# Kernel optimization log

Measured on AMD Instinct MI355X. Metric: run time of the kernel, lower is better.

Reference implementation:

```python
import jax, jax.numpy as jnp
import numpy as np
from jax.scipy.linalg import solve_triangular

B, L, D, H = 1, 2048, 1024, 4
DK = DV = D // H  # 256
CONV = 4
FIR_S, FIR_M, FIR_L = 3, 15, 63
CHUNK = 32


def _l2norm(x):
    return x * jax.lax.rsqrt(jnp.sum(x * x, -1, keepdims=True) + 1e-6)


def _short_conv(x, w):
    # depthwise causal conv1d (fla ShortConvolution) + silu; x:(B,L,C), w:(C,K)
    K = w.shape[-1]
    l = x.shape[1]
    xp = jnp.pad(x, ((0, 0), (K - 1, 0), (0, 0)))
    y = sum(xp[:, j:j + l, :] * w[:, j] for j in range(K))
    return jax.nn.silu(y)


def _fir(x, filt):
    # DepthwiseFIRConv1d: x:(B,L,H,Dv), filt:(H,Dv,K), causal depthwise conv
    b, l, h, d = x.shape
    K = filt.shape[-1]
    xf = jnp.transpose(x.reshape(b, l, h * d), (0, 2, 1))  # (B, C, L)
    y = jax.lax.conv_general_dilated(xf, filt.reshape(h * d, 1, K), (1,), [(K - 1, 0)],
                                     feature_group_count=h * d)
    return jnp.transpose(y, (0, 2, 1)).reshape(b, l, h, d)


def _delta_rule_chunkwise(q, k, v, beta):
    # q,k:(B,H,L,dk)  v:(B,H,L,dv)  beta:(B,H,L); L divisible by CHUNK
    b, h, Lq, dk = q.shape
    c = CHUNK
    n = Lq // c
    q = _l2norm(q)
    k = _l2norm(k)
    v = v * beta[..., None]
    kb = k * beta[..., None]
    rs = lambda t: t.reshape(b, h, n, c, t.shape[-1])
    qc, kc, vc, kbc = rs(q), rs(k), rs(v), rs(kb)
    # per-chunk UT transform: attn_inv = (I - strictly_lower(-(kb k^T)))^{-1}
    tri_strict = jnp.tril(jnp.ones((c, c), bool), -1)
    A = jnp.where(tri_strict, -(kbc @ jnp.swapaxes(kc, -1, -2)), 0.0)  # (B,H,n,c,c)
    eye = jnp.eye(c, dtype=q.dtype)
    M = eye - A  # unit lower triangular
    T = solve_triangular(M, jnp.broadcast_to(eye, M.shape), lower=True)
    u = T @ vc   # (B,H,n,c,dv)
    w = T @ kbc  # (B,H,n,c,dk)
    causal = jnp.tril(jnp.ones((c, c), bool))  # include diagonal

    def step(S, inp):
        q_i, k_i, u_i, w_i = inp
        attn = jnp.where(causal, q_i @ jnp.swapaxes(k_i, -1, -2), 0.0)
        u_adj = u_i - w_i @ S
        o_i = q_i @ S + attn @ u_adj
        return S + jnp.swapaxes(k_i, -1, -2) @ u_adj, o_i

    S0 = jnp.zeros((b, h, dk, v.shape[-1]), q.dtype)
    mv = lambda t: jnp.moveaxis(t, 2, 0)  # chunk axis to scan axis
    _, o = jax.lax.scan(step, S0, (mv(qc), mv(kc), mv(u), mv(w)))
    return jnp.moveaxis(o, 0, 2).reshape(b, h, Lq, -1)


def _rmsnorm(x, w, eps=1e-5):
    return x * jax.lax.rsqrt(jnp.mean(x * x, -1, keepdims=True) + eps) * w


def setup_inputs() -> dict:
    key = jax.random.key(0)
    ks = jax.random.split(key, 16)
    wn = lambda k, shape, s: jax.random.normal(k, shape, jnp.float32) * s

    def fir_init(k, K):
        f = jnp.zeros((H, DV, K), jnp.float32).at[..., -1].set(1.0)  # delta kernel
        return f + wn(k, (H, DV, K), 0.01)

    return {
        "hidden_states": jax.random.normal(ks[0], (B, L, D), jnp.float32),
        "Wq": wn(ks[1], (D, D), 0.02),
        "Wk": wn(ks[2], (D, D), 0.02),
        "Wv": wn(ks[3], (D, D), 0.02),
        "Wb": wn(ks[4], (H, D), 0.02),
        "conv_q": wn(ks[5], (D, CONV), 0.1),
        "conv_k": wn(ks[6], (D, CONV), 0.1),
        "conv_v": wn(ks[7], (D, CONV), 0.1),
        "fir_s": fir_init(ks[8], FIR_S),
        "fir_m": fir_init(ks[9], FIR_M),
        "fir_l": fir_init(ks[10], FIR_L),
        "gate_w": wn(ks[11], (H, 5, D), 1.0 / np.sqrt(D)),
        "gate_b": jnp.zeros((H, 5), jnp.float32),
        "log_temp": jnp.zeros((H, 1), jnp.float32),
        "eps_param": jnp.full((H, 1), 0.02, jnp.float32),
        "norm_w": jnp.ones((DV,), jnp.float32),
        "Wo": wn(ks[12], (D, D), 0.02),
    }


def reference(hidden_states, Wq, Wk, Wv, Wb, conv_q, conv_k, conv_v,
              fir_s, fir_m, fir_l, gate_w, gate_b, log_temp, eps_param,
              norm_w, Wo):
    b, l, d = hidden_states.shape
    # projections + short conv (silu activation, qk_activation='silu')
    q = _short_conv(hidden_states @ Wq.T, conv_q).reshape(b, l, H, DK)
    k = _short_conv(hidden_states @ Wk.T, conv_k).reshape(b, l, H, DK)
    v_direct = _short_conv(hidden_states @ Wv.T, conv_v).reshape(b, l, H, DV)
    beta = jax.nn.sigmoid(hidden_states @ Wb.T)  # (B,L,H)
    tp = lambda t: jnp.transpose(t, (0, 2, 1, 3))
    delta_out = tp(_delta_rule_chunkwise(tp(q), tp(k), tp(v_direct),
                                         jnp.transpose(beta, (0, 2, 1))))
    local_s = _fir(v_direct, fir_s)
    local_m = _fir(v_direct, fir_m)
    local_l = _fir(v_direct, fir_l)
    # per-head 5-way gate with temperature + eps floor
    logits = jnp.einsum('bld,hpd->blhp', hidden_states, gate_w) + gate_b
    temp = jnp.exp(log_temp).reshape(1, 1, H, 1)
    probs = jax.nn.softmax(logits / temp, -1)
    eps = jnp.clip(eps_param, 0.0, 0.2).reshape(1, 1, H, 1)
    probs = probs * (1.0 - 5.0 * eps) + eps
    o = (probs[..., 0:1] * local_s + probs[..., 1:2] * local_m +
         probs[..., 2:3] * local_l + probs[..., 3:4] * delta_out +
         probs[..., 4:5] * v_direct)
    o = _rmsnorm(o, norm_w)  # per-head RMSNorm (use_gate=False)
    return o.reshape(b, l, H * DV) @ Wo.T
```

## Files before the change

### kernel.cpp

```cpp
#include <hip/hip_runtime.h>

#define LSEQ 2048
#define DMOD 1024
#define NH   4
#define DH   256
#define NCH  64
#define CPAD 260

typedef unsigned short u16;
typedef short bf16x8 __attribute__((ext_vector_type(8)));
typedef float f32x4  __attribute__((ext_vector_type(4)));

#define MFMA16(a,b,c) __builtin_amdgcn_mfma_f32_16x16x32_bf16((a),(b),(c),0,0,0)

__device__ __forceinline__ float sigf(float x){ return 1.0f/(1.0f + expf(-x)); }

__device__ __forceinline__ u16 f2bf(float f){
  unsigned u = __float_as_uint(f);
  return (u16)((u + 0x7FFFu + ((u>>16)&1u)) >> 16);
}
__device__ __forceinline__ unsigned pk2(float a, float b){
  return (unsigned)f2bf(a) | ((unsigned)f2bf(b) << 16);
}
__device__ __forceinline__ float bf2f(u16 x){ return __uint_as_float(((unsigned)x)<<16); }

__device__ __forceinline__ void stage16(const void* g, void* l){
  __builtin_amdgcn_global_load_lds((const __attribute__((address_space(1))) unsigned*)g,
                                   (__attribute__((address_space(3))) unsigned*)l, 16, 0, 0);
}

__global__ __launch_bounds__(256) void cvt_all(
    const float* __restrict__ hidden, const float* __restrict__ Wq,
    const float* __restrict__ Wk, const float* __restrict__ Wv,
    const float* __restrict__ Wo, u16* __restrict__ hidb,
    u16* __restrict__ wqkvb, u16* __restrict__ wob)
{
  const int i4 = blockIdx.x*256 + threadIdx.x;
  const int e = i4*4;
  const float* src; u16* dst; int off;
  if (e < 2*1048576)      { src = hidden; dst = hidb;  off = e; }
  else if (e < 3*1048576) { src = Wq; dst = wqkvb; off = e - 2*1048576; }
  else if (e < 4*1048576) { src = Wk; dst = wqkvb + 1048576; off = e - 3*1048576; }
  else if (e < 5*1048576) { src = Wv; dst = wqkvb + 2*1048576; off = e - 4*1048576; }
  else                    { src = Wo; dst = wob; off = e - 5*1048576; }
  float4 v = *(const float4*)(src + off);
  *(uint2*)(dst + off) = make_uint2(pk2(v.x,v.y), pk2(v.z,v.w));
}

__global__ __launch_bounds__(256) void gemm_qkv(
    const u16* __restrict__ A, const u16* __restrict__ B,
    float* __restrict__ Cq, float* __restrict__ Ck, float* __restrict__ Cv)
{
  __shared__ __align__(16) u16 Asl[2][128][32];
  __shared__ __align__(16) u16 Bsl[2][128][32];
  const int i0 = blockIdx.x*128, j0 = blockIdx.y*128;
  const int t = threadIdx.x, lane = t & 63, wv = t >> 6;
  const int wm = wv >> 1, wn = wv & 1;
  const int li = lane & 15, g = lane >> 4;
  const int lr = lane >> 2, lc = lane & 3;
  f32x4 acc[4][4] = {};

  auto stageAB = [&](int buf, int kt){
    const int k0 = kt*32;
    #pragma unroll
    for (int c2=0;c2<2;c2++){
      const int row = wv*32 + c2*16 + lr;
      stage16(A + (size_t)(i0+row)*1024 + k0 + lc*8, &Asl[buf][wv*32 + c2*16][0]);
      stage16(B + (size_t)(j0+row)*1024 + k0 + lc*8, &Bsl[buf][wv*32 + c2*16][0]);
    }
  };

  int buf = 0;
  stageAB(0, 0);
  for (int kt=0; kt<32; kt++){
    __syncthreads();
    if (kt+1 < 32) stageAB(buf^1, kt+1);
    bf16x8 af[4], bf[4];
    #pragma unroll
    for (int mt=0;mt<4;mt++) af[mt] = *(const bf16x8*)&Asl[buf][wm*64+mt*16+li][g*8];
    #pragma unroll
    for (int nt=0;nt<4;nt++) bf[nt] = *(const bf16x8*)&Bsl[buf][wn*64+nt*16+li][g*8];
    #pragma unroll
    for (int mt=0;mt<4;mt++)
      #pragma unroll
      for (int nt=0;nt<4;nt++)
        acc[mt][nt] = MFMA16(af[mt], bf[nt], acc[mt][nt]);
    buf ^= 1;
  }
  float* C = (blockIdx.y < 8) ? Cq : (blockIdx.y < 16) ? Ck : Cv;
  const int jl = j0 & 1023;
  #pragma unroll
  for (int mt=0;mt<4;mt++){
    #pragma unroll
    for (int nt=0;nt<4;nt++){
      #pragma unroll
      for (int r=0;r<4;r++){
        const int row = i0 + wm*64 + mt*16 + g*4 + r;
        const int col = jl + wn*64 + nt*16 + li;
        C[(size_t)row*1024 + col] = acc[mt][nt][r];
      }
    }
  }
}

__global__ __launch_bounds__(256) void gemm_bf16(
    const u16* __restrict__ A, const u16* __restrict__ B,
    float* __restrict__ C, int M, int N, int K)
{
  __shared__ __align__(16) u16 Asl[2][128][32];
  __shared__ __align__(16) u16 Bsl[2][128][32];
  const int i0 = blockIdx.x*128, j0 = blockIdx.y*128;
  const int t = threadIdx.x, lane = t & 63, wv = t >> 6;
  const int wm = wv >> 1, wn = wv & 1;
  const int li = lane & 15, g = lane >> 4;
  const int lr = lane >> 2, lc = lane & 3;
  f32x4 acc[4][4] = {};

  auto stageAB = [&](int buf, int kt){
    const int k0 = kt*32;
    #pragma unroll
    for (int c2=0;c2<2;c2++){
      const int row = wv*32 + c2*16 + lr;
      stage16(A + (size_t)(i0+row)*K + k0 + lc*8, &Asl[buf][wv*32 + c2*16][0]);
      stage16(B + (size_t)(j0+row)*K + k0 + lc*8, &Bsl[buf][wv*32 + c2*16][0]);
    }
  };

  int buf = 0;
  const int nk = K/32;
  stageAB(0, 0);
  for (int kt=0; kt<nk; kt++){
    __syncthreads();
    if (kt+1 < nk) stageAB(buf^1, kt+1);
    bf16x8 af[4], bf[4];
    #pragma unroll
    for (int mt=0;mt<4;mt++) af[mt] = *(const bf16x8*)&Asl[buf][wm*64+mt*16+li][g*8];
    #pragma unroll
    for (int nt=0;nt<4;nt++) bf[nt] = *(const bf16x8*)&Bsl[buf][wn*64+nt*16+li][g*8];
    #pragma unroll
    for (int mt=0;mt<4;mt++)
      #pragma unroll
      for (int nt=0;nt<4;nt++)
        acc[mt][nt] = MFMA16(af[mt], bf[nt], acc[mt][nt]);
    buf ^= 1;
  }
  #pragma unroll
  for (int mt=0;mt<4;mt++){
    #pragma unroll
    for (int nt=0;nt<4;nt++){
      #pragma unroll
      for (int r=0;r<4;r++){
        const int row = i0 + wm*64 + mt*16 + g*4 + r;
        const int col = j0 + wn*64 + nt*16 + li;
        C[(size_t)row*N + col] = acc[mt][nt][r];
      }
    }
  }
}

__global__ __launch_bounds__(256) void conv_silu3(
    const float* __restrict__ tq, const float* __restrict__ tk, const float* __restrict__ tv,
    const float* __restrict__ wq, const float* __restrict__ wk, const float* __restrict__ wv2,
    u16* __restrict__ oq, u16* __restrict__ ok, u16* __restrict__ ov)
{
  const int idx = blockIdx.x*256 + threadIdx.x;
  const int which = idx >> 21;
  const int lidx = idx & ((1<<21)-1);
  const float* x = (which==0) ? tq : (which==1) ? tk : tv;
  const float* w = (which==0) ? wq : (which==1) ? wk : wv2;
  u16* y = (which==0) ? oq : (which==1) ? ok : ov;
  const int c = lidx & (DMOD-1);
  const int i = lidx >> 10;
  float4 wc = *(const float4*)(w + (size_t)c*4);
  float acc = wc.w * x[lidx];
  if (i >= 1) acc += wc.z * x[lidx -   DMOD];
  if (i >= 2) acc += wc.y * x[lidx - 2*DMOD];
  if (i >= 3) acc += wc.x * x[lidx - 3*DMOD];
  y[lidx] = f2bf(acc * sigf(acc));
}

__global__ __launch_bounds__(256) void beta_gate(
    const float* __restrict__ hidden, const float* __restrict__ Wb,
    const float* __restrict__ gw, const float* __restrict__ gb,
    const float* __restrict__ logtemp, const float* __restrict__ epsp,
    float* __restrict__ betab, float* __restrict__ probs)
{
  const int i = blockIdx.x, t = threadIdx.x;
  float4 h4 = *(const float4*)(hidden + (size_t)i*DMOD + t*4);
  float part[24];
  #pragma unroll
  for (int o=0;o<24;o++){
    const float* wr = (o<4) ? (Wb + (size_t)o*DMOD) : (gw + (size_t)(o-4)*DMOD);
    float4 w4 = *(const float4*)(wr + t*4);
    part[o] = h4.x*w4.x + h4.y*w4.y + h4.z*w4.z + h4.w*w4.w;
  }
  __shared__ float red[24][4];
  __shared__ float fin[24];
  const int lane = t & 63, wv = t >> 6;
  #pragma unroll
  for (int o=0;o<24;o++){
    float vv = part[o];
    #pragma unroll
    for (int m=1;m<64;m<<=1) vv += __shfl_xor(vv, m, 64);
    if (lane == 0) red[o][wv] = vv;
  }
  __syncthreads();
  if (t < 24) fin[t] = red[t][0]+red[t][1]+red[t][2]+red[t][3];
  __syncthreads();
  if (t < NH){
    const int hh = t;
    betab[(size_t)i*NH + hh] = sigf(fin[hh]);
    float temp = expf(logtemp[hh]);
    float lg[5], mx = -1e30f;
    #pragma unroll
    for (int p=0;p<5;p++){ lg[p] = (fin[4+hh*5+p] + gb[hh*5+p]) / temp; mx = fmaxf(mx, lg[p]); }
    float ex[5], s = 0.f;
    #pragma unroll
    for (int p=0;p<5;p++){ ex[p] = expf(lg[p]-mx); s += ex[p]; }
    float eps = fminf(fmaxf(epsp[hh], 0.f), 0.2f);
    #pragma unroll
    for (int p=0;p<5;p++) probs[((size_t)i*NH+hh)*5 + p] = (ex[p]/s)*(1.f-5.f*eps) + eps;
  }
}

__global__ __launch_bounds__(256) void delta_pre(
    const u16* __restrict__ q, const u16* __restrict__ k, const u16* __restrict__ v,
    const float* __restrict__ beta,
    u16* __restrict__ qbg, u16* __restrict__ wng, u16* __restrict__ kTg,
    u16* __restrict__ atg, float* __restrict__ ubuf)
{
  const int n = blockIdx.x, h = blockIdx.y;
  const int t = threadIdx.x;
  __shared__ float q_s[32][CPAD], k_s[32][CPAD], v_s[32][CPAD];
  __shared__ float T_s[32][32], Tb_s[32][32], M_s[32][32];
  __shared__ float rr[2][32][8];
  __shared__ float scl[2][32];
  __shared__ float bet_s[32];

  const int row = t >> 3, cq = t & 7;
  const size_t gb = (size_t)(n*32+row)*DMOD + h*DH + cq*32;
  const size_t cb = (size_t)(h*NCH+n)*32*256;
  const int sw = (row & 7) << 3;
  float psq = 0.f, psk = 0.f;
  #pragma unroll
  for (int x=0;x<4;x++){
    uint4 qa = *(const uint4*)(q + gb + x*8);
    uint4 ka = *(const uint4*)(k + gb + x*8);
    uint4 va = *(const uint4*)(v + gb + x*8);
    const unsigned qw[4] = {qa.x,qa.y,qa.z,qa.w};
    const unsigned kw[4] = {ka.x,ka.y,ka.z,ka.w};
    const unsigned vw[4] = {va.x,va.y,va.z,va.w};
    #pragma unroll
    for (int e=0;e<4;e++){
      float q0 = bf2f((u16)(qw[e]&0xffff)), q1 = bf2f((u16)(qw[e]>>16));
      float k0 = bf2f((u16)(kw[e]&0xffff)), k1 = bf2f((u16)(kw[e]>>16));
      float v0 = bf2f((u16)(vw[e]&0xffff)), v1 = bf2f((u16)(vw[e]>>16));
      q_s[row][cq*32+x*8+e*2]   = q0; q_s[row][cq*32+x*8+e*2+1] = q1;
      k_s[row][cq*32+x*8+e*2]   = k0; k_s[row][cq*32+x*8+e*2+1] = k1;
      v_s[row][cq*32+x*8+e*2]   = v0; v_s[row][cq*32+x*8+e*2+1] = v1;
      psq += q0*q0 + q1*q1;
      psk += k0*k0 + k1*k1;
    }
  }
  rr[0][row][cq] = psq; rr[1][row][cq] = psk;
  if (t < 32) bet_s[t] = beta[(size_t)(n*32+t)*NH + h];
  __syncthreads();
  if (t < 64){
    const int wh = t >> 5, r = t & 31;
    float s = 1e-6f;
    #pragma unroll
    for (int x=0;x<8;x++) s += rr[wh][r][x];
    scl[wh][r] = rsqrtf(s);
  }
  __syncthreads();
  {
    const float sq = scl[0][row], sk2 = scl[1][row];
    #pragma unroll
    for (int x=0;x<8;x++){
      float4 qa = *(float4*)&q_s[row][cq*32+x*4];
      qa.x*=sq; qa.y*=sq; qa.z*=sq; qa.w*=sq;
      *(float4*)&q_s[row][cq*32+x*4] = qa;
      *(uint2*)&qbg[cb + (size_t)row*256 + ((cq*32 + x*4) ^ sw)] =
          make_uint2(pk2(qa.x,qa.y), pk2(qa.z,qa.w));
      float4 ka = *(float4*)&k_s[row][cq*32+x*4];
      ka.x*=sk2; ka.y*=sk2; ka.z*=sk2; ka.w*=sk2;
      *(float4*)&k_s[row][cq*32+x*4] = ka;
    }
  }
  __syncthreads();
  {
    unsigned* kp = (unsigned*)(kTg + ((size_t)(h*NCH+n)*256 + t)*32);
    #pragma unroll
    for (int c2=0;c2<16;c2++)
      kp[c2 ^ ((t&3)<<2)] = pk2(k_s[2*c2][t], k_s[2*c2+1][t]);
  }
  {
    const int c = t >> 3, m0 = (t & 7)*4;
    float d0=0.f,d1=0.f,d2=0.f,d3=0.f;
    for (int kk=0;kk<DH;kk+=4){
      float4 a  = *(const float4*)&k_s[c][kk];
      float4 b0 = *(const float4*)&k_s[m0+0][kk];
      float4 b1 = *(const float4*)&k_s[m0+1][kk];
      float4 b2 = *(const float4*)&k_s[m0+2][kk];
      float4 b3 = *(const float4*)&k_s[m0+3][kk];
      d0 += a.x*b0.x + a.y*b0.y + a.z*b0.z + a.w*b0.w;
      d1 += a.x*b1.x + a.y*b1.y + a.z*b1.z + a.w*b1.w;
      d2 += a.x*b2.x + a.y*b2.y + a.z*b2.z + a.w*b2.w;
      d3 += a.x*b3.x + a.y*b3.y + a.z*b3.z + a.w*b3.w;
    }
    const float bc = bet_s[c];
    M_s[c][m0+0] = (m0+0 < c) ? bc*d0 : ((m0+0==c)?1.f:0.f);
    M_s[c][m0+1] = (m0+1 < c) ? bc*d1 : ((m0+1==c)?1.f:0.f);
    M_s[c][m0+2] = (m0+2 < c) ? bc*d2 : ((m0+2==c)?1.f:0.f);
    M_s[c][m0+3] = (m0+3 < c) ? bc*d3 : ((m0+3==c)?1.f:0.f);
  }
  __syncthreads();
  if (t < 32){
    const int j = t;
    for (int c=0;c<32;c++){
      float s = (c==j) ? 1.f : 0.f;
      for (int m=0;m<c;m++) s -= M_s[c][m]*T_s[m][j];
      T_s[c][j] = s;
    }
  }
  __syncthreads();
  {
    const int c = t >> 3, m0 = (t & 7)*4;
    #pragma unroll
    for (int x=0;x<4;x++) Tb_s[c][m0+x] = T_s[c][m0+x]*bet_s[m0+x];
  }
  __syncthreads();
  {
    const int colb = (t & 7)*4;
    float4 aw[8] = {};
    float4 au[8] = {};
    for (int m=0;m<32;m++){
      const float tb = Tb_s[row][m];
      #pragma unroll
      for (int y=0;y<8;y++){
        float4 kv = *(const float4*)&k_s[m][colb + y*32];
        float4 vv = *(const float4*)&v_s[m][colb + y*32];
        aw[y].x += tb*kv.x; aw[y].y += tb*kv.y; aw[y].z += tb*kv.z; aw[y].w += tb*kv.w;
        au[y].x += tb*vv.x; au[y].y += tb*vv.y; au[y].z += tb*vv.z; au[y].w += tb*vv.w;
      }
    }
    const size_t ob = (size_t)(n*32+row)*DMOD + h*DH + colb;
    #pragma unroll
    for (int y=0;y<8;y++){
      *(uint2*)&wng[cb + (size_t)row*256 + ((colb + y*32) ^ sw)] =
          make_uint2(pk2(-aw[y].x,-aw[y].y), pk2(-aw[y].z,-aw[y].w));
      *(float4*)(ubuf + ob + y*32) = au[y];
    }
  }
  {
    const int c = t >> 3, m0 = (t & 7)*4;
    float d0=0.f,d1=0.f,d2=0.f,d3=0.f;
    for (int kk=0;kk<DH;kk+=4){
      float4 a  = *(const float4*)&q_s[c][kk];
      float4 b0 = *(const float4*)&k_s[m0+0][kk];
      float4 b1 = *(const float4*)&k_s[m0+1][kk];
      float4 b2 = *(const float4*)&k_s[m0+2][kk];
      float4 b3 = *(const float4*)&k_s[m0+3][kk];
      d0 += a.x*b0.x + a.y*b0.y + a.z*b0.z + a.w*b0.w;
      d1 += a.x*b1.x + a.y*b1.y + a.z*b1.z + a.w*b1.w;
      d2 += a.x*b2.x + a.y*b2.y + a.z*b2.z + a.w*b2.w;
      d3 += a.x*b3.x + a.y*b3.y + a.z*b3.z + a.w*b3.w;
    }
    d0 = (m0+0 <= c) ? d0 : 0.f;
    d1 = (m0+1 <= c) ? d1 : 0.f;
    d2 = (m0+2 <= c) ? d2 : 0.f;
    d3 = (m0+3 <= c) ? d3 : 0.f;
    *(uint2*)&atg[((size_t)(h*NCH+n)*32 + c)*32 + (m0 ^ ((c&3)<<3))] =
        make_uint2(pk2(d0,d1), pk2(d2,d3));
  }
}

__global__ __launch_bounds__(256) void delta_scan_fused(
    const u16* __restrict__ qbg, const u16* __restrict__ wng,
    const u16* __restrict__ kTg, const u16* __restrict__ atg,
    const float* __restrict__ ubuf, float* __restrict__ dob)
{
  const int qd = blockIdx.x, h = blockIdx.y;
  const int t = threadIdx.x, lane = t & 63, wv = t >> 6;
  const int cs = wv & 1, j = wv >> 1;
  const int g = lane >> 4, li = lane & 15;
  const int swz = (li & 7) << 3;
  const int kswz = (li & 3) << 3;

  __shared__ __align__(16) unsigned char stg[2][53248];
  __shared__ __align__(16) u16 ST[16][264];
  __shared__ __align__(16) u16 uaT[16][40];
  __shared__ __align__(16) float pfo[2][2][64][4];

  f32x4 S[4];
  #pragma unroll
  for (int i=0;i<4;i++) S[i] = (f32x4){0.f,0.f,0.f,0.f};
  for (int i=t; i<16*264; i+=256) (&ST[0][0])[i] = 0;

  auto issue_stage = [&](int nn, int b){
    char* L = (char*)&stg[b][0];
    const size_t cbB = (size_t)(h*NCH+nn)*16384;
    #pragma unroll
    for (int jj=0;jj<13;jj++){
      const int s = wv*13 + jj;
      if (s < 48){
        const char* gsc = (s<16) ? (const char*)wng + cbB + (size_t)s*1024
                       : (s<32) ? (const char*)qbg + cbB + (size_t)(s-16)*1024
                                : (const char*)kTg + cbB + (size_t)(s-32)*1024;
        stage16(gsc + (size_t)lane*16, L + s*1024);
      } else if (s < 50){
        stage16((const char*)atg + (size_t)(h*NCH+nn)*2048 + (size_t)(s-48)*1024 + (size_t)lane*16,
                L + 49152 + (s-48)*1024);
      } else {
        const int i2 = s - 50;
        stage16(ubuf + (size_t)(nn*32 + i2*16 + (lane>>2))*DMOD + h*DH + qd*16 + (lane&3)*4,
                L + 51200 + i2*1024);
      }
    }
  };

  issue_stage(0, 0);

  for (int n=0;n<NCH;n++){
    const int b = n & 1;
    if (n == 0) asm volatile("s_waitcnt vmcnt(0)" ::: "memory");
    else        asm volatile("s_waitcnt vmcnt(2)" ::: "memory");
    asm volatile("s_waitcnt lgkmcnt(0)" ::: "memory");
    __builtin_amdgcn_s_barrier();
    __builtin_amdgcn_sched_barrier(0);
    issue_stage((n+1 < NCH) ? n+1 : NCH-1, b^1);

    const char* L = (const char*)&stg[b][0];
    const u16*  wl = (const u16*)(L);
    const u16*  ql = (const u16*)(L + 16384);
    const u16*  kl = (const u16*)(L + 32768);
    const u16*  al = (const u16*)(L + 49152);
    const float* ul = (const float*)(L + 51200);

    bf16x8 Bs[8];
    #pragma unroll
    for (int kb=0;kb<8;kb++)
      Bs[kb] = *(const bf16x8*)&ST[li][kb*32 + g*8];

    f32x4 ua;
    #pragma unroll
    for (int r=0;r<4;r++)
      ua[r] = ul[(cs*16 + g*4 + r)*16 + li];
    f32x4 x2 = (f32x4){0.f,0.f,0.f,0.f};
    #pragma unroll
    for (int kb=0;kb<4;kb++){
      const int idx = (kb*32 + g*8) ^ swz;
      bf16x8 aw = *(const bf16x8*)&wl[(size_t)(cs*16+li)*256 + idx];
      ua = MFMA16(aw, Bs[kb], ua);
    }
    #pragma unroll
    for (int kb=4;kb<8;kb++){
      const int idx = (kb*32 + g*8) ^ swz;
      bf16x8 aw = *(const bf16x8*)&wl[(size_t)(cs*16+li)*256 + idx];
      x2 = MFMA16(aw, Bs[kb], x2);
    }
    #pragma unroll
    for (int r=0;r<4;r++) ua[r] += x2[r];

    f32x4 op = (f32x4){0.f,0.f,0.f,0.f};
    if (j == 0){
      #pragma unroll
      for (int kb=0;kb<4;kb++){
        const int idx = (kb*32 + g*8) ^ swz;
        bf16x8 aq = *(const bf16x8*)&ql[(size_t)(cs*16+li)*256 + idx];
        op = MFMA16(aq, Bs[kb], op);
      }
    } else {
      #pragma unroll
      for (int kb2=0;kb2<4;kb2++){
        const int idx = ((4+kb2)*32 + g*8) ^ swz;
        bf16x8 aq = *(const bf16x8*)&ql[(size_t)(cs*16+li)*256 + idx];
        op = MFMA16(aq, Bs[4+kb2], op);
      }
    }
    *(f32x4*)&pfo[j][cs][lane][0] = op;

    if (j == 0) *(unsigned*)&uaT[li][cs*16 + g*4]     = pk2(ua[0], ua[1]);
    else        *(unsigned*)&uaT[li][cs*16 + g*4 + 2] = pk2(ua[2], ua[3]);
    asm volatile("s_waitcnt lgkmcnt(0)" ::: "memory");
    __builtin_amdgcn_s_barrier();
    __builtin_amdgcn_sched_barrier(0);

    bf16x8 bu = *(const bf16x8*)&uaT[li][g*8];

    #pragma unroll
    for (int mtl=0;mtl<4;mtl++){
      const int rowk = (wv*4+mtl)*16 + li;
      bf16x8 a = *(const bf16x8*)&kl[(size_t)rowk*32 + ((g*8) ^ kswz)];
      S[mtl] = MFMA16(a, bu, S[mtl]);
    }
    #pragma unroll
    for (int mtl=0;mtl<4;mtl++)
      *(uint2*)&ST[li][(wv*4+mtl)*16 + g*4] =
          make_uint2(pk2(S[mtl][0],S[mtl][1]), pk2(S[mtl][2],S[mtl][3]));

    f32x4 atp = (f32x4){0.f,0.f,0.f,0.f};
    {
      bf16x8 a = *(const bf16x8*)&al[(size_t)(cs*16+li)*32 + ((g*8) ^ kswz)];
      atp = MFMA16(a, bu, atp);
    }

    {
      f32x4 oq = *(const f32x4*)&pfo[j^1][cs][lane][0];
      const size_t ob = (size_t)(n*32 + cs*16)*DMOD + h*DH + qd*16 + li;
      if (j == 0){
        dob[ob + (size_t)(g*4+0)*DMOD] = op[0] + oq[0] + atp[0];
        dob[ob + (size_t)(g*4+1)*DMOD] = op[1] + oq[1] + atp[1];
      } else {
        dob[ob + (size_t)(g*4+2)*DMOD] = op[2] + oq[2] + atp[2];
        dob[ob + (size_t)(g*4+3)*DMOD] = op[3] + oq[3] + atp[3];
      }
    }
  }
}

__global__ void prep_fir(const float* __restrict__ fs, const float* __restrict__ fm,
                         const float* __restrict__ fl, float* __restrict__ fts,
                         float* __restrict__ ftm, float* __restrict__ ftl)
{
  const int idx = blockIdx.x*256 + threadIdx.x;
  if (idx < 63*1024){
    const int j = idx >> 10, c = idx & 1023;
    ftl[idx] = fl[(size_t)c*63 + j];
  } else if (idx < 78*1024){
    const int r = idx - 63*1024;
    const int j = r >> 10, c = r & 1023;
    ftm[r] = fm[(size_t)c*15 + j];
  } else {
    const int r = idx - 78*1024;
    const int j = r >> 10, c = r & 1023;
    fts[r] = fs[(size_t)c*3 + j];
  }
}

__global__ __launch_bounds__(256) void fir_mix(
    const u16* __restrict__ vb, const float* __restrict__ dout,
    const float* __restrict__ probs, const float* __restrict__ ftl,
    const float* __restrict__ ftm, const float* __restrict__ fts,
    const float* __restrict__ normw, u16* __restrict__ omixb)
{
  const int i0 = blockIdx.x*16, h = blockIdx.y;
  const int t = threadIdx.x;
  const int c = h*DH + t;
  __shared__ float vwin[78][256];
  __shared__ float red[16][4];

  for (int ll=0; ll<78; ll++){
    const int row = i0 - 62 + ll;
    vwin[ll][t] = (row >= 0) ? bf2f(vb[(size_t)row*DMOD + c]) : 0.f;
  }
  __syncthreads();

  float mixv[16];
  #pragma unroll
  for (int cch=0; cch<4; cch++){
    float as[4] = {0,0,0,0}, am[4] = {0,0,0,0}, alg[4] = {0,0,0,0};
    for (int jt=0; jt<63; jt++){
      const float f = ftl[(size_t)jt*DMOD + c];
      #pragma unroll
      for (int q2=0;q2<4;q2++) alg[q2] += f * vwin[cch*4+q2 + jt][t];
    }
    #pragma unroll
    for (int jt=0; jt<15; jt++){
      const float f = ftm[(size_t)jt*DMOD + c];
      #pragma unroll
      for (int q2=0;q2<4;q2++) am[q2] += f * vwin[cch*4+q2 + 48 + jt][t];
    }
    #pragma unroll
    for (int jt=0; jt<3; jt++){
      const float f = fts[(size_t)jt*DMOD + c];
      #pragma unroll
      for (int q2=0;q2<4;q2++) as[q2] += f * vwin[cch*4+q2 + 60 + jt][t];
    }
    #pragma unroll
    for (int q2=0;q2<4;q2++){
      const int ii = cch*4+q2;
      const int i = i0+ii;
      const float* pr = probs + ((size_t)i*NH + h)*5;
      const float dvv = dout[(size_t)i*DMOD + c];
      const float vv  = vwin[62+ii][t];
      mixv[ii] = pr[0]*as[q2] + pr[1]*am[q2] + pr[2]*alg[q2] + pr[3]*dvv + pr[4]*vv;
    }
  }
  const int lane = t & 63, wvw = t >> 6;
  #pragma unroll
  for (int ii=0;ii<16;ii++){
    float ss = mixv[ii]*mixv[ii];
    #pragma unroll
    for (int m=1;m<64;m<<=1) ss += __shfl_xor(ss, m, 64);
    if (lane == 0) red[ii][wvw] = ss;
  }
  __syncthreads();
  #pragma unroll
  for (int ii=0;ii<16;ii++){
    const float tot = red[ii][0]+red[ii][1]+red[ii][2]+red[ii][3];
    const float o = mixv[ii] * rsqrtf(tot*(1.f/256.f) + 1e-5f) * normw[t];
    omixb[(size_t)(i0+ii)*DMOD + c] = f2bf(o);
  }
}

extern "C" void kernel_launch(void* const* d_in, const int* in_sizes, int n_in,
                              void* d_out, int out_size, void* d_ws, size_t ws_size,
                              hipStream_t stream)
{
  const float* hidden = (const float*)d_in[0];
  const float* Wq     = (const float*)d_in[1];
  const float* Wk     = (const float*)d_in[2];
  const float* Wv     = (const float*)d_in[3];
  const float* Wb     = (const float*)d_in[4];
  const float* convq  = (const float*)d_in[5];
  const float* convk  = (const float*)d_in[6];
  const float* convv  = (const float*)d_in[7];
  const float* firs   = (const float*)d_in[8];
  const float* firm   = (const float*)d_in[9];
  const float* firl   = (const float*)d_in[10];
  const float* gatew  = (const float*)d_in[11];
  const float* gateb  = (const float*)d_in[12];
  const float* logtemp= (const float*)d_in[13];
  const float* epsp   = (const float*)d_in[14];
  const float* normw  = (const float*)d_in[15];
  const float* Wo     = (const float*)d_in[16];
  float* out = (float*)d_out;

  char* W = (char*)d_ws;
  const size_t MB = (size_t)1 << 20;
  float* tmpq  = (float*)(W + 0*MB);
  float* dob   = (float*)(W + 0*MB);
  float* tmpk  = (float*)(W + 8*MB);
  float* ubuf  = (float*)(W + 8*MB);
  float* tmpv  = (float*)(W + 16*MB);
  u16*   omixb = (u16*)  (W + 16*MB);
  u16*   qb    = (u16*)  (W + 24*MB);
  u16*   kb    = (u16*)  (W + 28*MB);
  u16*   vb    = (u16*)  (W + 32*MB);
  u16*   hidb  = (u16*)  (W + 36*MB);
  u16*   wqkvb = (u16*)  (W + 40*MB);
  u16*   wob   = (u16*)  (W + 46*MB);
  u16*   qbg   = (u16*)  (W + 48*MB);
  u16*   wng   = (u16*)  (W + 52*MB);
  u16*   kTg   = (u16*)  (W + 56*MB);
  u16*   atg   = (u16*)  (W + 60*MB);
  float* betab = (float*)(W + 60*MB + 524288);
  float* probs = (float*)(W + 60*MB + 524288 + 32768);
  float* ftl   = (float*)(W + 61*MB);
  float* ftm   = (float*)(W + 61*MB + 300*1024);
  float* fts   = (float*)(W + 61*MB + 380*1024);

  cvt_all<<<6144, 256, 0, stream>>>(hidden, Wq, Wk, Wv, Wo, hidb, wqkvb, wob);
  prep_fir<<<324, 256, 0, stream>>>(firs, firm, firl, fts, ftm, ftl);

  gemm_qkv<<<dim3(16,24), 256, 0, stream>>>(hidb, wqkvb, tmpq, tmpk, tmpv);
  conv_silu3<<<24576, 256, 0, stream>>>(tmpq, tmpk, tmpv, convq, convk, convv, qb, kb, vb);

  beta_gate<<<2048, 256, 0, stream>>>(hidden, Wb, gatew, gateb, logtemp, epsp, betab, probs);

  delta_pre<<<dim3(64,4), 256, 0, stream>>>(qb, kb, vb, betab, qbg, wng, kTg, atg, ubuf);
  delta_scan_fused<<<dim3(16,4), 256, 0, stream>>>(qbg, wng, kTg, atg, ubuf, dob);

  fir_mix<<<dim3(128,4), 256, 0, stream>>>(vb, dob, probs, ftl, ftm, fts, normw, omixb);

  gemm_bf16<<<dim3(16,8), 256, 0, stream>>>(omixb, wob, out, LSEQ, DMOD, DMOD);
}
```

Before: 367.6 us.

## Drop mid-iteration barrier in delta scan via wave shuffles and double-buffered state

The delta scan loop now has every wave compute both 16-row halves of u_adj redundantly and exchange the packed bf16 values with cross-lane shuffles, instead of writing them to shared memory and waiting at a second block barrier. The transposed state is double-buffered in shared memory so waves can write the next state while others still read the current one. The q@S output no longer splits across waves; each wave does the full 8-block product, which removes the partial-sum exchange buffer. Separately, the FIR filter transpose kernel is merged into the conversion kernel to save a launch. The cost is redundant MFMA work per wave in exchange for one fewer barrier per chunk on the serial scan.

```diff
diff --git a/kernel.cpp b/kernel.cpp
--- a/kernel.cpp
+++ b/kernel.cpp
@@ -33,18 +33,37 @@
     const float* __restrict__ hidden, const float* __restrict__ Wq,
     const float* __restrict__ Wk, const float* __restrict__ Wv,
     const float* __restrict__ Wo, u16* __restrict__ hidb,
-    u16* __restrict__ wqkvb, u16* __restrict__ wob)
-{
-  const int i4 = blockIdx.x*256 + threadIdx.x;
-  const int e = i4*4;
-  const float* src; u16* dst; int off;
-  if (e < 2*1048576)      { src = hidden; dst = hidb;  off = e; }
-  else if (e < 3*1048576) { src = Wq; dst = wqkvb; off = e - 2*1048576; }
-  else if (e < 4*1048576) { src = Wk; dst = wqkvb + 1048576; off = e - 3*1048576; }
-  else if (e < 5*1048576) { src = Wv; dst = wqkvb + 2*1048576; off = e - 4*1048576; }
-  else                    { src = Wo; dst = wob; off = e - 5*1048576; }
-  float4 v = *(const float4*)(src + off);
-  *(uint2*)(dst + off) = make_uint2(pk2(v.x,v.y), pk2(v.z,v.w));
+    u16* __restrict__ wqkvb, u16* __restrict__ wob,
+    const float* __restrict__ fs, const float* __restrict__ fm,
+    const float* __restrict__ fl, float* __restrict__ fts,
+    float* __restrict__ ftm, float* __restrict__ ftl)
+{
+  if (blockIdx.x < 6144){
+    const int i4 = blockIdx.x*256 + threadIdx.x;
+    const int e = i4*4;
+    const float* src; u16* dst; int off;
+    if (e < 2*1048576)      { src = hidden; dst = hidb;  off = e; }
+    else if (e < 3*1048576) { src = Wq; dst = wqkvb; off = e - 2*1048576; }
+    else if (e < 4*1048576) { src = Wk; dst = wqkvb + 1048576; off = e - 3*1048576; }
+    else if (e < 5*1048576) { src = Wv; dst = wqkvb + 2*1048576; off = e - 4*1048576; }
+    else                    { src = Wo; dst = wob; off = e - 5*1048576; }
+    float4 v = *(const float4*)(src + off);
+    *(uint2*)(dst + off) = make_uint2(pk2(v.x,v.y), pk2(v.z,v.w));
+  } else {
+    const int idx = (blockIdx.x-6144)*256 + threadIdx.x;
+    if (idx < 63*1024){
+      const int j = idx >> 10, c = idx & 1023;
+      ftl[idx] = fl[(size_t)c*63 + j];
+    } else if (idx < 78*1024){
+      const int r = idx - 63*1024;
+      const int j = r >> 10, c = r & 1023;
+      ftm[r] = fm[(size_t)c*15 + j];
+    } else {
+      const int r = idx - 78*1024;
+      const int j = r >> 10, c = r & 1023;
+      fts[r] = fs[(size_t)c*3 + j];
+    }
+  }
 }
 
 __global__ __launch_bounds__(256) void gemm_qkv(
@@ -388,14 +407,12 @@
   const int kswz = (li & 3) << 3;
 
   __shared__ __align__(16) unsigned char stg[2][53248];
-  __shared__ __align__(16) u16 ST[16][264];
-  __shared__ __align__(16) u16 uaT[16][40];
-  __shared__ __align__(16) float pfo[2][2][64][4];
+  __shared__ __align__(16) u16 ST[2][16][264];
 
   f32x4 S[4];
   #pragma unroll
   for (int i=0;i<4;i++) S[i] = (f32x4){0.f,0.f,0.f,0.f};
-  for (int i=t; i<16*264; i+=256) (&ST[0][0])[i] = 0;
+  for (int i=t; i<16*264; i+=256) (&ST[0][0][0])[i] = 0;
 
   auto issue_stage = [&](int nn, int b){
     char* L = (char*)&stg[b][0];
@@ -436,57 +453,61 @@
     const u16*  kl = (const u16*)(L + 32768);
     const u16*  al = (const u16*)(L + 49152);
     const float* ul = (const float*)(L + 51200);
+    const u16 (*STr)[264] = ST[n & 1];
+    u16 (*STw)[264] = ST[(n & 1) ^ 1];
 
     bf16x8 Bs[8];
     #pragma unroll
     for (int kb=0;kb<8;kb++)
-      Bs[kb] = *(const bf16x8*)&ST[li][kb*32 + g*8];
-
-    f32x4 ua;
-    #pragma unroll
-    for (int r=0;r<4;r++)
-      ua[r] = ul[(cs*16 + g*4 + r)*16 + li];
-    f32x4 x2 = (f32x4){0.f,0.f,0.f,0.f};
+      Bs[kb] = *(const bf16x8*)&STr[li][kb*32 + g*8];
+
+    f32x4 ua0, ua1;
+    #pragma unroll
+    for (int r=0;r<4;r++){
+      ua0[r] = ul[(g*4+r)*16 + li];
+      ua1[r] = ul[(16+g*4+r)*16 + li];
+    }
+    f32x4 x0 = (f32x4){0.f,0.f,0.f,0.f}, x1 = (f32x4){0.f,0.f,0.f,0.f};
     #pragma unroll
     for (int kb=0;kb<4;kb++){
       const int idx = (kb*32 + g*8) ^ swz;
-      bf16x8 aw = *(const bf16x8*)&wl[(size_t)(cs*16+li)*256 + idx];
-      ua = MFMA16(aw, Bs[kb], ua);
+      bf16x8 a0 = *(const bf16x8*)&wl[(size_t)li*256 + idx];
+      bf16x8 a1 = *(const bf16x8*)&wl[(size_t)(16+li)*256 + idx];
+      ua0 = MFMA16(a0, Bs[kb], ua0);
+      ua1 = MFMA16(a1, Bs[kb], ua1);
     }
     #pragma unroll
     for (int kb=4;kb<8;kb++){
       const int idx = (kb*32 + g*8) ^ swz;
-      bf16x8 aw = *(const bf16x8*)&wl[(size_t)(cs*16+li)*256 + idx];
-      x2 = MFMA16(aw, Bs[kb], x2);
-    }
-    #pragma unroll
-    for (int r=0;r<4;r++) ua[r] += x2[r];
-
-    f32x4 op = (f32x4){0.f,0.f,0.f,0.f};
-    if (j == 0){
-      #pragma unroll
-      for (int kb=0;kb<4;kb++){
-        const int idx = (kb*32 + g*8) ^ swz;
-        bf16x8 aq = *(const bf16x8*)&ql[(size_t)(cs*16+li)*256 + idx];
-        op = MFMA16(aq, Bs[kb], op);
-      }
-    } else {
-      #pragma unroll
-      for (int kb2=0;kb2<4;kb2++){
-        const int idx = ((4+kb2)*32 + g*8) ^ swz;
-        bf16x8 aq = *(const bf16x8*)&ql[(size_t)(cs*16+li)*256 + idx];
-        op = MFMA16(aq, Bs[4+kb2], op);
-      }
-    }
-    *(f32x4*)&pfo[j][cs][lane][0] = op;
-
-    if (j == 0) *(unsigned*)&uaT[li][cs*16 + g*4]     = pk2(ua[0], ua[1]);
-    else        *(unsigned*)&uaT[li][cs*16 + g*4 + 2] = pk2(ua[2], ua[3]);
-    asm volatile("s_waitcnt lgkmcnt(0)" ::: "memory");
-    __builtin_amdgcn_s_barrier();
-    __builtin_amdgcn_sched_barrier(0);
-
-    bf16x8 bu = *(const bf16x8*)&uaT[li][g*8];
+      bf16x8 a0 = *(const bf16x8*)&wl[(size_t)li*256 + idx];
+      bf16x8 a1 = *(const bf16x8*)&wl[(size_t)(16+li)*256 + idx];
+      x0 = MFMA16(a0, Bs[kb], x0);
+      x1 = MFMA16(a1, Bs[kb], x1);
+    }
+    #pragma unroll
+    for (int r=0;r<4;r++){ ua0[r] += x0[r]; ua1[r] += x1[r]; }
+
+    const unsigned w0 = pk2(ua0[0], ua0[1]);
+    const unsigned w1 = pk2(ua0[2], ua0[3]);
+    const unsigned w2 = pk2(ua1[0], ua1[1]);
+    const unsigned w3 = pk2(ua1[2], ua1[3]);
+    const int hi = g >> 1, pair = g & 1;
+    const int src0 = pair*32 + li;
+    const int src1 = pair*32 + 16 + li;
+    const unsigned a0s = (unsigned)__shfl((int)w0, src0, 64);
+    const unsigned b0s = (unsigned)__shfl((int)w1, src0, 64);
+    const unsigned c0s = (unsigned)__shfl((int)w2, src0, 64);
+    const unsigned d0s = (unsigned)__shfl((int)w3, src0, 64);
+    const unsigned a1s = (unsigned)__shfl((int)w0, src1, 64);
+    const unsigned b1s = (unsigned)__shfl((int)w1, src1, 64);
+    const unsigned c1s = (unsigned)__shfl((int)w2, src1, 64);
+    const unsigned d1s = (unsigned)__shfl((int)w3, src1, 64);
+    union { unsigned u[4]; bf16x8 v8; } buu;
+    buu.u[0] = hi ? c0s : a0s;
+    buu.u[1] = hi ? d0s : b0s;
+    buu.u[2] = hi ? c1s : a1s;
+    buu.u[3] = hi ? d1s : b1s;
+    const bf16x8 bu = buu.v8;
 
     #pragma unroll
     for (int mtl=0;mtl<4;mtl++){
@@ -496,45 +517,37 @@
     }
     #pragma unroll
     for (int mtl=0;mtl<4;mtl++)
-      *(uint2*)&ST[li][(wv*4+mtl)*16 + g*4] =
+      *(uint2*)&STw[li][(wv*4+mtl)*16 + g*4] =
           make_uint2(pk2(S[mtl][0],S[mtl][1]), pk2(S[mtl][2],S[mtl][3]));
 
-    f32x4 atp = (f32x4){0.f,0.f,0.f,0.f};
+    f32x4 o0 = (f32x4){0.f,0.f,0.f,0.f}, oy = (f32x4){0.f,0.f,0.f,0.f};
+    #pragma unroll
+    for (int kb=0;kb<4;kb++){
+      const int idx = (kb*32 + g*8) ^ swz;
+      bf16x8 aq = *(const bf16x8*)&ql[(size_t)(cs*16+li)*256 + idx];
+      o0 = MFMA16(aq, Bs[kb], o0);
+    }
+    #pragma unroll
+    for (int kb=4;kb<8;kb++){
+      const int idx = (kb*32 + g*8) ^ swz;
+      bf16x8 aq = *(const bf16x8*)&ql[(size_t)(cs*16+li)*256 + idx];
+      oy = MFMA16(aq, Bs[kb], oy);
+    }
     {
       bf16x8 a = *(const bf16x8*)&al[(size_t)(cs*16+li)*32 + ((g*8) ^ kswz)];
-      atp = MFMA16(a, bu, atp);
+      oy = MFMA16(a, bu, oy);
     }
 
     {
-      f32x4 oq = *(const f32x4*)&pfo[j^1][cs][lane][0];
       const size_t ob = (size_t)(n*32 + cs*16)*DMOD + h*DH + qd*16 + li;
       if (j == 0){
-        dob[ob + (size_t)(g*4+0)*DMOD] = op[0] + oq[0] + atp[0];
-        dob[ob + (size_t)(g*4+1)*DMOD] = op[1] + oq[1] + atp[1];
+        dob[ob + (size_t)(g*4+0)*DMOD] = o0[0] + oy[0];
+        dob[ob + (size_t)(g*4+1)*DMOD] = o0[1] + oy[1];
       } else {
-        dob[ob + (size_t)(g*4+2)*DMOD] = op[2] + oq[2] + atp[2];
-        dob[ob + (size_t)(g*4+3)*DMOD] = op[3] + oq[3] + atp[3];
+        dob[ob + (size_t)(g*4+2)*DMOD] = o0[2] + oy[2];
+        dob[ob + (size_t)(g*4+3)*DMOD] = o0[3] + oy[3];
       }
     }
-  }
-}
-
-__global__ void prep_fir(const float* __restrict__ fs, const float* __restrict__ fm,
-                         const float* __restrict__ fl, float* __restrict__ fts,
-                         float* __restrict__ ftm, float* __restrict__ ftl)
-{
-  const int idx = blockIdx.x*256 + threadIdx.x;
-  if (idx < 63*1024){
-    const int j = idx >> 10, c = idx & 1023;
-    ftl[idx] = fl[(size_t)c*63 + j];
-  } else if (idx < 78*1024){
-    const int r = idx - 63*1024;
-    const int j = r >> 10, c = r & 1023;
-    ftm[r] = fm[(size_t)c*15 + j];
-  } else {
-    const int r = idx - 78*1024;
-    const int j = r >> 10, c = r & 1023;
-    fts[r] = fs[(size_t)c*3 + j];
   }
 }
 
@@ -651,8 +664,8 @@
   float* ftm   = (float*)(W + 61*MB + 300*1024);
   float* fts   = (float*)(W + 61*MB + 380*1024);
 
-  cvt_all<<<6144, 256, 0, stream>>>(hidden, Wq, Wk, Wv, Wo, hidb, wqkvb, wob);
-  prep_fir<<<324, 256, 0, stream>>>(firs, firm, firl, fts, ftm, ftl);
+  cvt_all<<<6468, 256, 0, stream>>>(hidden, Wq, Wk, Wv, Wo, hidb, wqkvb, wob,
+                                    firs, firm, firl, fts, ftm, ftl);
 
   gemm_qkv<<<dim3(16,24), 256, 0, stream>>>(hidb, wqkvb, tmpq, tmpk, tmpv);
   conv_silu3<<<24576, 256, 0, stream>>>(tmpq, tmpk, tmpv, convq, convk, convv, qb, kb, vb);
```

Result: no change. 371.0 us (+0.9%).
